# Optimization experiments

Measured on AMD Instinct MI355X. Metric: run time of the kernel, lower is better.

## Reference

```python
import jax, jax.numpy as jnp
import numpy as np


def _conv1x1(x, w, b):
    # x: [B,C,H,W], w: [O,C], b: [O] -> [B,O,H,W]
    return jnp.einsum('bchw,oc->bohw', x, w) + b[None, :, None, None]


def setup_inputs() -> dict:
    key = jax.random.key(0)
    ks = jax.random.split(key, 5)
    B, C, H, W = 4, 256, 64, 64
    C2 = C // 2
    scale = 0.02  # keep attention logits in a sane range
    return {
        'x': jax.random.normal(ks[0], (B, C, H, W), dtype=jnp.float32),
        'w_theta': jax.random.normal(ks[1], (C2, C), dtype=jnp.float32) * scale,
        'b_theta': jnp.zeros((C2,), dtype=jnp.float32),
        'w_phi': jax.random.normal(ks[2], (C2, C), dtype=jnp.float32) * scale,
        'b_phi': jnp.zeros((C2,), dtype=jnp.float32),
        'w_g': jax.random.normal(ks[3], (C2, C), dtype=jnp.float32) * scale,
        'b_g': jnp.zeros((C2,), dtype=jnp.float32),
        'w_out': jax.random.normal(ks[4], (C, C2), dtype=jnp.float32) * scale,
        'b_out': jnp.zeros((C,), dtype=jnp.float32),
    }


def reference(x, w_theta, b_theta, w_phi, b_phi, w_g, b_g, w_out, b_out):
    B, C, H, W = x.shape
    C2 = C // 2
    N = H * W
    theta = _conv1x1(x, w_theta, b_theta).reshape(B, C2, N)  # [B,C2,N]
    phi = _conv1x1(x, w_phi, b_phi).reshape(B, C2, N)        # [B,C2,N]
    g = _conv1x1(x, w_g, b_g).reshape(B, C2, N)              # [B,C2,N]
    # non-local attention: scores[b,m,n] = theta[b,:,m] . phi[b,:,n]
    scores = jnp.einsum('bcm,bcn->bmn', theta, phi)          # [B,N,N]
    attn = jax.nn.softmax(scores, axis=-1)                   # [B,N,N]
    # output = g @ attn^T : out[b,c,m] = sum_n g[b,c,n] * attn[b,m,n]
    out = jnp.einsum('bcn,bmn->bcm', g, attn)                # [B,C2,N]
    out = out.reshape(B, C2, H, W)
    return x + _conv1x1(out, w_out, b_out)
```

## Files before the change

kernel.cpp:

```cpp
#include <hip/hip_runtime.h>
#include <hip/hip_bf16.h>

#define B_  4
#define C_  256
#define C2_ 128
#define N_  4096
#define LOG2E 1.4426950408889634f

typedef unsigned short u16;
typedef __attribute__((ext_vector_type(8))) short bf16x8;
typedef __attribute__((ext_vector_type(4))) float f32x4;

static __device__ __forceinline__ u16 f2bf(float f) {
    return __builtin_bit_cast(u16, __float2bfloat16(f));
}
static __device__ __forceinline__ float bf2f(u16 u) {
    return __bfloat162float(__builtin_bit_cast(__hip_bfloat16, u));
}

__global__ __launch_bounds__(256) void prep_kernel(
    const float* __restrict__ wt, const float* __restrict__ wp,
    const float* __restrict__ wg, const float* __restrict__ wo,
    const float* __restrict__ x, u16* __restrict__ Wb, u16* __restrict__ XT) {
    __shared__ float T[64][65];
    int bid = blockIdx.x;
    int tid = threadIdx.x;
    if (bid < 128) {
        int i = (bid * 256 + tid) * 4;
        int mat = i >> 15, off = i & 32767;
        const float* src = mat == 0 ? wt : (mat == 1 ? wp : (mat == 2 ? wg : wo));
        float4 v = *(const float4*)(src + off);
        ushort4 o = { f2bf(v.x), f2bf(v.y), f2bf(v.z), f2bf(v.w) };
        *(ushort4*)(Wb + i) = o;
        return;
    }
    int bid2 = bid - 128;
    int b   = bid2 / (4 * 64);
    int rem = bid2 % (4 * 64);
    int c0  = (rem / 64) * 64;
    int n0  = (rem % 64) * 64;
#pragma unroll
    for (int it = 0; it < 4; ++it) {
        int idx = it * 256 + tid;
        int rc = idx >> 4, n4 = (idx & 15) * 4;
        float4 v = *(const float4*)(x + ((size_t)b * C_ + c0 + rc) * N_ + n0 + n4);
        T[n4 + 0][rc] = v.x;
        T[n4 + 1][rc] = v.y;
        T[n4 + 2][rc] = v.z;
        T[n4 + 3][rc] = v.w;
    }
    __syncthreads();
#pragma unroll
    for (int it = 0; it < 2; ++it) {
        int idx = it * 256 + tid;
        int nr = idx >> 3, c8 = (idx & 7) * 8;
        u16 o[8];
#pragma unroll
        for (int j = 0; j < 8; ++j) o[j] = f2bf(T[nr][c8 + j]);
        *(uint4*)(XT + ((size_t)b * N_ + n0 + nr) * C_ + c0 + c8) = *(const uint4*)o;
    }
}

__global__ __launch_bounds__(256) void projm_kernel(
    const u16* __restrict__ XT, const u16* __restrict__ Wb,
    const float* __restrict__ b_theta, const float* __restrict__ b_phi,
    const float* __restrict__ b_g,
    u16* __restrict__ Q, u16* __restrict__ K, u16* __restrict__ V) {
    __shared__ __align__(16) u16 XTs[64][264];
    __shared__ __align__(16) u16 Vt[128][72];
    int bid = blockIdx.x;
    int mat = bid / (B_ * (N_ / 64));
    int rem = bid % (B_ * (N_ / 64));
    int b   = rem / (N_ / 64);
    int n0  = (rem % (N_ / 64)) * 64;
    int tid = threadIdx.x;
    int wave = tid >> 6, lane = tid & 63, quad = lane >> 4, l16 = lane & 15;

#pragma unroll
    for (int it = 0; it < 8; ++it) {
        int idx = it * 256 + tid;
        int row = idx >> 5, c8 = (idx & 31) * 8;
        *(uint4*)&XTs[row][c8] =
            *(const uint4*)(XT + ((size_t)b * N_ + n0 + row) * C_ + c8);
    }
    __syncthreads();

    bf16x8 af[8];
#pragma unroll
    for (int ks = 0; ks < 8; ++ks)
        af[ks] = *(const bf16x8*)&XTs[wave * 16 + l16][ks * 32 + quad * 8];

    const u16* wm = Wb + (size_t)mat * C2_ * C_;
    const float* bias = mat == 0 ? b_theta : (mat == 1 ? b_phi : b_g);

    f32x4 acc[8];
#pragma unroll
    for (int i = 0; i < 8; ++i) acc[i] = (f32x4){0.f, 0.f, 0.f, 0.f};
#pragma unroll
    for (int ct = 0; ct < 8; ++ct) {
        const u16* wr = wm + (size_t)(ct * 16 + l16) * C_ + quad * 8;
#pragma unroll
        for (int ks = 0; ks < 8; ++ks) {
            bf16x8 bf = *(const bf16x8*)(wr + ks * 32);
            acc[ct] = __builtin_amdgcn_mfma_f32_16x16x32_bf16(af[ks], bf, acc[ct], 0, 0, 0);
        }
    }

    if (mat < 2) {
        u16* dst = mat == 0 ? Q : K;
        float sc = mat == 0 ? LOG2E : 1.0f;
#pragma unroll
        for (int ct = 0; ct < 8; ++ct) {
            float bb = bias[ct * 16 + l16];
#pragma unroll
            for (int r = 0; r < 4; ++r) {
                int n = n0 + wave * 16 + quad * 4 + r;
                dst[((size_t)b * N_ + n) * C2_ + ct * 16 + l16] =
                    f2bf((acc[ct][r] + bb) * sc);
            }
        }
    } else {
#pragma unroll
        for (int ct = 0; ct < 8; ++ct) {
            float bb = bias[ct * 16 + l16];
#pragma unroll
            for (int r = 0; r < 4; ++r)
                Vt[ct * 16 + l16][wave * 16 + quad * 4 + r] = f2bf(acc[ct][r] + bb);
        }
        __syncthreads();
#pragma unroll
        for (int it = 0; it < 4; ++it) {
            int idx = it * 256 + tid;
            int row = idx >> 3, n8 = (idx & 7) * 8;
            *(uint4*)(V + ((size_t)b * C2_ + row) * N_ + n0 + n8) =
                *(const uint4*)&Vt[row][n8];
        }
    }
}

__global__ __launch_bounds__(256, 2) void attn_kernel(
    const u16* __restrict__ Q, const u16* __restrict__ K,
    const u16* __restrict__ V, u16* __restrict__ AO,
    float* __restrict__ Op, float* __restrict__ lsum, int nsplit) {
    const int BM = 128, BN = 64, D = C2_;
    const int per = B_ * (N_ / BM);
    int s    = blockIdx.x / per;
    int r0   = blockIdx.x % per;
    int b    = r0 / (N_ / BM);
    int m0   = (r0 % (N_ / BM)) * BM;
    int tid  = threadIdx.x;
    int wave = tid >> 6, lane = tid & 63, quad = (lane >> 4) & 3, l16 = lane & 15;

    __shared__ __align__(16) u16 Ks[BN][D + 8];
    __shared__ __align__(16) u16 Vs[D][BN + 8];
    __shared__ __align__(16) u16 Psb[4][32][BN + 8];
    u16* Ps = &Psb[wave][0][0];

    bf16x8 qf[2][4];
#pragma unroll
    for (int ms = 0; ms < 2; ++ms) {
        const u16* qp = Q + ((size_t)b * N_ + m0 + wave * 32 + ms * 16 + l16) * D;
#pragma unroll
        for (int kk = 0; kk < 4; ++kk)
            qf[ms][kk] = *(const bf16x8*)(qp + kk * 32 + quad * 8);
    }

    float l_r[2][4] = {{0.f, 0.f, 0.f, 0.f}, {0.f, 0.f, 0.f, 0.f}};
    f32x4 o_acc[2][8];
#pragma unroll
    for (int ms = 0; ms < 2; ++ms)
#pragma unroll
        for (int i = 0; i < 8; ++i) o_acc[ms][i] = (f32x4){0.f, 0.f, 0.f, 0.f};

    const int chunk = N_ / nsplit;
    const int nt0 = s * chunk, nt1 = nt0 + chunk;

    for (int nt = nt0; nt < nt1; nt += BN) {
        const u16* kp = K + ((size_t)b * N_ + nt) * D;
#pragma unroll
        for (int it = 0; it < 4; ++it) {
            int idx = it * 256 + tid;
            int row = idx >> 4, col = (idx & 15) * 8;
            *(uint4*)&Ks[row][col] = *(const uint4*)(kp + row * D + col);
        }
#pragma unroll
        for (int it = 0; it < 4; ++it) {
            int idx = it * 256 + tid;
            int row = idx >> 3, col = (idx & 7) * 8;
            *(uint4*)&Vs[row][col] =
                *(const uint4*)(V + ((size_t)b * C2_ + row) * N_ + nt + col);
        }
        __syncthreads();

        f32x4 sc[2][4];
#pragma unroll
        for (int nn = 0; nn < 4; ++nn) {
            f32x4 a0 = (f32x4){0.f, 0.f, 0.f, 0.f};
            f32x4 a1 = (f32x4){0.f, 0.f, 0.f, 0.f};
#pragma unroll
            for (int kk = 0; kk < 4; ++kk) {
                bf16x8 kf = *(const bf16x8*)&Ks[nn * 16 + l16][kk * 32 + quad * 8];
                a0 = __builtin_amdgcn_mfma_f32_16x16x32_bf16(qf[0][kk], kf, a0, 0, 0, 0);
                a1 = __builtin_amdgcn_mfma_f32_16x16x32_bf16(qf[1][kk], kf, a1, 0, 0, 0);
            }
            sc[0][nn] = a0;
            sc[1][nn] = a1;
        }

#pragma unroll
        for (int ms = 0; ms < 2; ++ms)
#pragma unroll
            for (int nn = 0; nn < 4; ++nn)
#pragma unroll
                for (int r = 0; r < 4; ++r) {
                    float p = __builtin_amdgcn_exp2f(sc[ms][nn][r]);
                    l_r[ms][r] += p;
                    Ps[(ms * 16 + quad * 4 + r) * (BN + 8) + nn * 16 + l16] = f2bf(p);
                }

#pragma unroll
        for (int ks = 0; ks < 2; ++ks) {
            bf16x8 pf0 = *(const bf16x8*)&Ps[(l16) * (BN + 8) + ks * 32 + quad * 8];
            bf16x8 pf1 = *(const bf16x8*)&Ps[(16 + l16) * (BN + 8) + ks * 32 + quad * 8];
#pragma unroll
            for (int cs = 0; cs < 8; ++cs) {
                bf16x8 vf = *(const bf16x8*)&Vs[cs * 16 + l16][ks * 32 + quad * 8];
                o_acc[0][cs] = __builtin_amdgcn_mfma_f32_16x16x32_bf16(pf0, vf, o_acc[0][cs], 0, 0, 0);
                o_acc[1][cs] = __builtin_amdgcn_mfma_f32_16x16x32_bf16(pf1, vf, o_acc[1][cs], 0, 0, 0);
            }
        }
        __syncthreads();
    }

#pragma unroll
    for (int ms = 0; ms < 2; ++ms)
#pragma unroll
        for (int r = 0; r < 4; ++r) {
            l_r[ms][r] += __shfl_xor(l_r[ms][r], 1);
            l_r[ms][r] += __shfl_xor(l_r[ms][r], 2);
            l_r[ms][r] += __shfl_xor(l_r[ms][r], 4);
            l_r[ms][r] += __shfl_xor(l_r[ms][r], 8);
        }

    if (Op) {
#pragma unroll
        for (int ms = 0; ms < 2; ++ms) {
#pragma unroll
            for (int cs = 0; cs < 8; ++cs)
#pragma unroll
                for (int r = 0; r < 4; ++r) {
                    size_t row = (size_t)s * (B_ * N_) + (size_t)b * N_ +
                                 m0 + wave * 32 + ms * 16 + quad * 4 + r;
                    Op[row * C2_ + cs * 16 + l16] = o_acc[ms][cs][r];
                }
            if (l16 == 0)
#pragma unroll
                for (int r = 0; r < 4; ++r) {
                    size_t row = (size_t)s * (B_ * N_) + (size_t)b * N_ +
                                 m0 + wave * 32 + ms * 16 + quad * 4 + r;
                    lsum[row] = l_r[ms][r];
                }
        }
    } else {
#pragma unroll
        for (int ms = 0; ms < 2; ++ms)
#pragma unroll
            for (int cs = 0; cs < 8; ++cs)
#pragma unroll
                for (int r = 0; r < 4; ++r) {
                    float v = o_acc[ms][cs][r] / l_r[ms][r];
                    AO[((size_t)b * N_ + m0 + wave * 32 + ms * 16 + quad * 4 + r) * C2_ +
                       cs * 16 + l16] = f2bf(v);
                }
    }
}

__global__ __launch_bounds__(256) void outproj_kernel(
    const float* __restrict__ x, const float* __restrict__ Op,
    const float* __restrict__ lsum, const u16* __restrict__ AO,
    const u16* __restrict__ Wob, const float* __restrict__ b_out,
    float* __restrict__ y, int nsplit) {
    __shared__ __align__(16) u16 As[64][C2_ + 8];
    __shared__ float Ls[64];
    int bid = blockIdx.x;
    int per_b = (C_ / 64) * (N_ / 64);
    int b   = bid / per_b;
    int rem = bid % per_b;
    int c0  = (rem / (N_ / 64)) * 64;
    int n0  = (rem % (N_ / 64)) * 64;
    int tid = threadIdx.x;
    int wave = tid >> 6, lane = tid & 63, quad = lane >> 4, l16 = lane & 15;

    if (nsplit > 1) {
        if (tid < 64) {
            float L = 0.f;
            for (int s = 0; s < nsplit; ++s)
                L += lsum[(size_t)s * (B_ * N_) + (size_t)b * N_ + n0 + tid];
            Ls[tid] = 1.f / L;
        }
        __syncthreads();
#pragma unroll
        for (int it = 0; it < 8; ++it) {
            int idx = it * 256 + tid;
            int n = idx >> 5, c4 = (idx & 31) * 4;
            float4 a = {0.f, 0.f, 0.f, 0.f};
            for (int s = 0; s < nsplit; ++s) {
                float4 v = *(const float4*)(
                    Op + ((size_t)s * (B_ * N_) + (size_t)b * N_ + n0 + n) * C2_ + c4);
                a.x += v.x; a.y += v.y; a.z += v.z; a.w += v.w;
            }
            float inv = Ls[n];
            ushort4 o = { f2bf(a.x * inv), f2bf(a.y * inv),
                          f2bf(a.z * inv), f2bf(a.w * inv) };
            *(ushort4*)&As[n][c4] = o;
        }
    } else {
#pragma unroll
        for (int it = 0; it < 4; ++it) {
            int idx = it * 256 + tid;
            int n = idx >> 4, c8 = (idx & 15) * 8;
            *(uint4*)&As[n][c8] =
                *(const uint4*)(AO + ((size_t)b * N_ + n0 + n) * C2_ + c8);
        }
    }
    __syncthreads();

    int cw = c0 + wave * 16;
    bf16x8 af[4];
#pragma unroll
    for (int kk = 0; kk < 4; ++kk)
        af[kk] = *(const bf16x8*)&Wob[(size_t)(cw + l16) * C2_ + kk * 32 + quad * 8];

    f32x4 acc[4];
#pragma unroll
    for (int i = 0; i < 4; ++i) acc[i] = (f32x4){0.f, 0.f, 0.f, 0.f};

#pragma unroll
    for (int nn = 0; nn < 4; ++nn)
#pragma unroll
        for (int kk = 0; kk < 4; ++kk) {
            bf16x8 bf = *(const bf16x8*)&As[nn * 16 + l16][kk * 32 + quad * 8];
            acc[nn] = __builtin_amdgcn_mfma_f32_16x16x32_bf16(af[kk], bf, acc[nn], 0, 0, 0);
        }

    float bo[4];
#pragma unroll
    for (int r = 0; r < 4; ++r) bo[r] = b_out[cw + quad * 4 + r];

#pragma unroll
    for (int nn = 0; nn < 4; ++nn)
#pragma unroll
        for (int r = 0; r < 4; ++r) {
            int c = cw + quad * 4 + r;
            size_t off = ((size_t)b * C_ + c) * N_ + n0 + nn * 16 + l16;
            y[off] = x[off] + bo[r] + acc[nn][r];
        }
}

extern "C" void kernel_launch(void* const* d_in, const int* in_sizes, int n_in,
                              void* d_out, int out_size, void* d_ws, size_t ws_size,
                              hipStream_t stream) {
    const float* x       = (const float*)d_in[0];
    const float* w_theta = (const float*)d_in[1];
    const float* b_theta = (const float*)d_in[2];
    const float* w_phi   = (const float*)d_in[3];
    const float* b_phi   = (const float*)d_in[4];
    const float* w_g     = (const float*)d_in[5];
    const float* b_g     = (const float*)d_in[6];
    const float* w_out   = (const float*)d_in[7];
    const float* b_out   = (const float*)d_in[8];
    float* y = (float*)d_out;

    const size_t SZ = (size_t)B_ * N_ * C2_;
    u16* Q  = (u16*)d_ws;
    u16* K  = Q + SZ;
    u16* V  = K + SZ;
    u16* AO = V + SZ;
    u16* Wb = AO + SZ;
    u16* Wob = Wb + (size_t)3 * C2_ * C_;
    u16* XT = Wb + (size_t)4 * C2_ * C_;
    char* dyn = (char*)(XT + (size_t)B_ * N_ * C_);
    size_t fixedB = (size_t)(dyn - (char*)d_ws);

    size_t perS = SZ * 4 + (size_t)B_ * N_ * 4;

    int S;
    if      (ws_size >= fixedB + 4 * perS) S = 4;
    else if (ws_size >= fixedB + 2 * perS) S = 2;
    else                                   S = 1;

    float* Op = nullptr;
    float* ls = nullptr;
    if (S > 1) {
        Op = (float*)dyn;
        ls = Op + (size_t)S * SZ;
    }

    prep_kernel<<<128 + B_ * (C_ / 64) * (N_ / 64), 256, 0, stream>>>(
        w_theta, w_phi, w_g, w_out, x, Wb, XT);
    projm_kernel<<<3 * B_ * (N_ / 64), 256, 0, stream>>>(
        XT, Wb, b_theta, b_phi, b_g, Q, K, V);
    attn_kernel<<<B_ * (N_ / 128) * S, 256, 0, stream>>>(Q, K, V, AO, Op, ls, S);
    outproj_kernel<<<B_ * (C_ / 64) * (N_ / 64), 256, 0, stream>>>(
        x, Op, ls, AO, Wob, b_out, y, S);
}
```

Baseline: 179.2 us.

## Fuse x transpose into projection, store split partials in bf16, allow six splits

The x transpose and bf16 conversion now happen inside a single projection kernel. That kernel computes Q, K and V together from one shared-memory tile of 32 positions, which removes the XT intermediate buffer and the separate transpose pass. The split-KV partial outputs are now stored as bf16 instead of fp32, halving that traffic, and up to six splits are allowed with uneven tile distribution. The bf16 partials lose some precision before the cross-split reduction, and the projection now runs 512 blocks instead of 768.

```diff
diff --git a/kernel.cpp b/kernel.cpp
--- a/kernel.cpp
+++ b/kernel.cpp
@@ -18,130 +18,114 @@
     return __bfloat162float(__builtin_bit_cast(__hip_bfloat16, u));
 }
 
-__global__ __launch_bounds__(256) void prep_kernel(
+__global__ __launch_bounds__(256) void prepw_kernel(
     const float* __restrict__ wt, const float* __restrict__ wp,
     const float* __restrict__ wg, const float* __restrict__ wo,
-    const float* __restrict__ x, u16* __restrict__ Wb, u16* __restrict__ XT) {
-    __shared__ float T[64][65];
-    int bid = blockIdx.x;
-    int tid = threadIdx.x;
-    if (bid < 128) {
-        int i = (bid * 256 + tid) * 4;
-        int mat = i >> 15, off = i & 32767;
-        const float* src = mat == 0 ? wt : (mat == 1 ? wp : (mat == 2 ? wg : wo));
-        float4 v = *(const float4*)(src + off);
-        ushort4 o = { f2bf(v.x), f2bf(v.y), f2bf(v.z), f2bf(v.w) };
-        *(ushort4*)(Wb + i) = o;
-        return;
-    }
-    int bid2 = bid - 128;
-    int b   = bid2 / (4 * 64);
-    int rem = bid2 % (4 * 64);
-    int c0  = (rem / 64) * 64;
-    int n0  = (rem % 64) * 64;
-#pragma unroll
-    for (int it = 0; it < 4; ++it) {
-        int idx = it * 256 + tid;
-        int rc = idx >> 4, n4 = (idx & 15) * 4;
-        float4 v = *(const float4*)(x + ((size_t)b * C_ + c0 + rc) * N_ + n0 + n4);
-        T[n4 + 0][rc] = v.x;
-        T[n4 + 1][rc] = v.y;
-        T[n4 + 2][rc] = v.z;
-        T[n4 + 3][rc] = v.w;
-    }
-    __syncthreads();
-#pragma unroll
-    for (int it = 0; it < 2; ++it) {
-        int idx = it * 256 + tid;
-        int nr = idx >> 3, c8 = (idx & 7) * 8;
-        u16 o[8];
-#pragma unroll
-        for (int j = 0; j < 8; ++j) o[j] = f2bf(T[nr][c8 + j]);
-        *(uint4*)(XT + ((size_t)b * N_ + n0 + nr) * C_ + c0 + c8) = *(const uint4*)o;
-    }
-}
-
-__global__ __launch_bounds__(256) void projm_kernel(
-    const u16* __restrict__ XT, const u16* __restrict__ Wb,
+    u16* __restrict__ Wb) {
+    int i = (blockIdx.x * 256 + threadIdx.x) * 4;
+    int mat = i >> 15, off = i & 32767;
+    const float* src = mat == 0 ? wt : (mat == 1 ? wp : (mat == 2 ? wg : wo));
+    float4 v = *(const float4*)(src + off);
+    ushort4 o = { f2bf(v.x), f2bf(v.y), f2bf(v.z), f2bf(v.w) };
+    *(ushort4*)(Wb + i) = o;
+}
+
+__global__ __launch_bounds__(256) void projx_kernel(
+    const float* __restrict__ x, const u16* __restrict__ Wb,
     const float* __restrict__ b_theta, const float* __restrict__ b_phi,
     const float* __restrict__ b_g,
     u16* __restrict__ Q, u16* __restrict__ K, u16* __restrict__ V) {
-    __shared__ __align__(16) u16 XTs[64][264];
-    __shared__ __align__(16) u16 Vt[128][72];
+    __shared__ __align__(16) union {
+        u16 XTs[32][264];
+        u16 Vt[128][40];
+    } sm;
     int bid = blockIdx.x;
-    int mat = bid / (B_ * (N_ / 64));
-    int rem = bid % (B_ * (N_ / 64));
-    int b   = rem / (N_ / 64);
-    int n0  = (rem % (N_ / 64)) * 64;
+    int b   = bid / (N_ / 32);
+    int n0  = (bid % (N_ / 32)) * 32;
     int tid = threadIdx.x;
     int wave = tid >> 6, lane = tid & 63, quad = lane >> 4, l16 = lane & 15;
-
-#pragma unroll
-    for (int it = 0; it < 8; ++it) {
+    int mgrp = wave >> 1, chalf = wave & 1;
+
+#pragma unroll
+    for (int it = 0; it < 4; ++it) {
         int idx = it * 256 + tid;
-        int row = idx >> 5, c8 = (idx & 31) * 8;
-        *(uint4*)&XTs[row][c8] =
-            *(const uint4*)(XT + ((size_t)b * N_ + n0 + row) * C_ + c8);
+        int q = idx & 7, p = idx >> 3;
+        const float* r0 = x + ((size_t)b * C_ + 2 * p) * N_ + n0 + 4 * q;
+        float4 v0 = *(const float4*)r0;
+        float4 v1 = *(const float4*)(r0 + N_);
+        const float* f0 = (const float*)&v0;
+        const float* f1 = (const float*)&v1;
+#pragma unroll
+        for (int j = 0; j < 4; ++j) {
+            unsigned pk = (unsigned)f2bf(f0[j]) | ((unsigned)f2bf(f1[j]) << 16);
+            *(unsigned*)&sm.XTs[4 * q + j][2 * p] = pk;
+        }
     }
     __syncthreads();
 
     bf16x8 af[8];
 #pragma unroll
     for (int ks = 0; ks < 8; ++ks)
-        af[ks] = *(const bf16x8*)&XTs[wave * 16 + l16][ks * 32 + quad * 8];
-
-    const u16* wm = Wb + (size_t)mat * C2_ * C_;
-    const float* bias = mat == 0 ? b_theta : (mat == 1 ? b_phi : b_g);
-
-    f32x4 acc[8];
-#pragma unroll
-    for (int i = 0; i < 8; ++i) acc[i] = (f32x4){0.f, 0.f, 0.f, 0.f};
-#pragma unroll
-    for (int ct = 0; ct < 8; ++ct) {
-        const u16* wr = wm + (size_t)(ct * 16 + l16) * C_ + quad * 8;
-#pragma unroll
-        for (int ks = 0; ks < 8; ++ks) {
-            bf16x8 bf = *(const bf16x8*)(wr + ks * 32);
-            acc[ct] = __builtin_amdgcn_mfma_f32_16x16x32_bf16(af[ks], bf, acc[ct], 0, 0, 0);
-        }
-    }
-
-    if (mat < 2) {
-        u16* dst = mat == 0 ? Q : K;
-        float sc = mat == 0 ? LOG2E : 1.0f;
-#pragma unroll
-        for (int ct = 0; ct < 8; ++ct) {
-            float bb = bias[ct * 16 + l16];
-#pragma unroll
-            for (int r = 0; r < 4; ++r) {
-                int n = n0 + wave * 16 + quad * 4 + r;
-                dst[((size_t)b * N_ + n) * C2_ + ct * 16 + l16] =
-                    f2bf((acc[ct][r] + bb) * sc);
-            }
-        }
-    } else {
-#pragma unroll
-        for (int ct = 0; ct < 8; ++ct) {
-            float bb = bias[ct * 16 + l16];
-#pragma unroll
-            for (int r = 0; r < 4; ++r)
-                Vt[ct * 16 + l16][wave * 16 + quad * 4 + r] = f2bf(acc[ct][r] + bb);
-        }
-        __syncthreads();
-#pragma unroll
-        for (int it = 0; it < 4; ++it) {
-            int idx = it * 256 + tid;
-            int row = idx >> 3, n8 = (idx & 7) * 8;
-            *(uint4*)(V + ((size_t)b * C2_ + row) * N_ + n0 + n8) =
-                *(const uint4*)&Vt[row][n8];
-        }
+        af[ks] = *(const bf16x8*)&sm.XTs[mgrp * 16 + l16][ks * 32 + quad * 8];
+    __syncthreads();
+
+    const float* biases[3] = { b_theta, b_phi, b_g };
+#pragma unroll
+    for (int mat = 0; mat < 3; ++mat) {
+        const u16* wm = Wb + (size_t)mat * C2_ * C_;
+        const float* bias = biases[mat];
+        f32x4 acc[4];
+#pragma unroll
+        for (int i = 0; i < 4; ++i) acc[i] = (f32x4){0.f, 0.f, 0.f, 0.f};
+#pragma unroll
+        for (int ct = 0; ct < 4; ++ct) {
+            int ce = chalf * 4 + ct;
+            const u16* wr = wm + (size_t)(ce * 16 + l16) * C_ + quad * 8;
+#pragma unroll
+            for (int ks = 0; ks < 8; ++ks) {
+                bf16x8 bf = *(const bf16x8*)(wr + ks * 32);
+                acc[ct] = __builtin_amdgcn_mfma_f32_16x16x32_bf16(af[ks], bf, acc[ct], 0, 0, 0);
+            }
+        }
+        if (mat < 2) {
+            u16* dst = mat == 0 ? Q : K;
+            float sc = mat == 0 ? LOG2E : 1.0f;
+#pragma unroll
+            for (int ct = 0; ct < 4; ++ct) {
+                int c2 = (chalf * 4 + ct) * 16 + l16;
+                float bb = bias[c2];
+#pragma unroll
+                for (int r = 0; r < 4; ++r) {
+                    int n = n0 + mgrp * 16 + quad * 4 + r;
+                    dst[((size_t)b * N_ + n) * C2_ + c2] = f2bf((acc[ct][r] + bb) * sc);
+                }
+            }
+        } else {
+#pragma unroll
+            for (int ct = 0; ct < 4; ++ct) {
+                int c2 = (chalf * 4 + ct) * 16 + l16;
+                float bb = bias[c2];
+#pragma unroll
+                for (int r = 0; r < 4; ++r)
+                    sm.Vt[c2][mgrp * 16 + quad * 4 + r] = f2bf(acc[ct][r] + bb);
+            }
+        }
+    }
+    __syncthreads();
+    {
+        int row = tid >> 1, col16 = (tid & 1) * 16;
+        uint4 a0 = *(const uint4*)&sm.Vt[row][col16];
+        uint4 a1 = *(const uint4*)&sm.Vt[row][col16 + 8];
+        u16* vp = V + ((size_t)b * C2_ + row) * N_ + n0 + col16;
+        *(uint4*)vp = a0;
+        *(uint4*)(vp + 8) = a1;
     }
 }
 
 __global__ __launch_bounds__(256, 2) void attn_kernel(
     const u16* __restrict__ Q, const u16* __restrict__ K,
     const u16* __restrict__ V, u16* __restrict__ AO,
-    float* __restrict__ Op, float* __restrict__ lsum, int nsplit) {
+    u16* __restrict__ Opb, float* __restrict__ lsum, int nsplit) {
     const int BM = 128, BN = 64, D = C2_;
     const int per = B_ * (N_ / BM);
     int s    = blockIdx.x / per;
@@ -172,8 +156,11 @@
 #pragma unroll
         for (int i = 0; i < 8; ++i) o_acc[ms][i] = (f32x4){0.f, 0.f, 0.f, 0.f};
 
-    const int chunk = N_ / nsplit;
-    const int nt0 = s * chunk, nt1 = nt0 + chunk;
+    const int tiles = N_ / BN;
+    const int base = tiles / nsplit, rem = tiles % nsplit;
+    const int t0 = s * base + (s < rem ? s : rem);
+    const int cnt = base + (s < rem ? 1 : 0);
+    const int nt0 = t0 * BN, nt1 = (t0 + cnt) * BN;
 
     for (int nt = nt0; nt < nt1; nt += BN) {
         const u16* kp = K + ((size_t)b * N_ + nt) * D;
@@ -242,7 +229,7 @@
             l_r[ms][r] += __shfl_xor(l_r[ms][r], 8);
         }
 
-    if (Op) {
+    if (Opb) {
 #pragma unroll
         for (int ms = 0; ms < 2; ++ms) {
 #pragma unroll
@@ -251,7 +238,7 @@
                 for (int r = 0; r < 4; ++r) {
                     size_t row = (size_t)s * (B_ * N_) + (size_t)b * N_ +
                                  m0 + wave * 32 + ms * 16 + quad * 4 + r;
-                    Op[row * C2_ + cs * 16 + l16] = o_acc[ms][cs][r];
+                    Opb[row * C2_ + cs * 16 + l16] = f2bf(o_acc[ms][cs][r]);
                 }
             if (l16 == 0)
 #pragma unroll
@@ -276,7 +263,7 @@
 }
 
 __global__ __launch_bounds__(256) void outproj_kernel(
-    const float* __restrict__ x, const float* __restrict__ Op,
+    const float* __restrict__ x, const u16* __restrict__ Opb,
     const float* __restrict__ lsum, const u16* __restrict__ AO,
     const u16* __restrict__ Wob, const float* __restrict__ b_out,
     float* __restrict__ y, int nsplit) {
@@ -300,19 +287,23 @@
         }
         __syncthreads();
 #pragma unroll
-        for (int it = 0; it < 8; ++it) {
+        for (int it = 0; it < 4; ++it) {
             int idx = it * 256 + tid;
-            int n = idx >> 5, c4 = (idx & 31) * 4;
-            float4 a = {0.f, 0.f, 0.f, 0.f};
+            int n = idx >> 4, c8 = (idx & 15) * 8;
+            float a[8] = {0.f, 0.f, 0.f, 0.f, 0.f, 0.f, 0.f, 0.f};
             for (int s = 0; s < nsplit; ++s) {
-                float4 v = *(const float4*)(
-                    Op + ((size_t)s * (B_ * N_) + (size_t)b * N_ + n0 + n) * C2_ + c4);
-                a.x += v.x; a.y += v.y; a.z += v.z; a.w += v.w;
+                const u16* op = Opb +
+                    ((size_t)s * (B_ * N_) + (size_t)b * N_ + n0 + n) * C2_ + c8;
+                uint4 raw = *(const uint4*)op;
+                const u16* rp = (const u16*)&raw;
+#pragma unroll
+                for (int j = 0; j < 8; ++j) a[j] += bf2f(rp[j]);
             }
             float inv = Ls[n];
-            ushort4 o = { f2bf(a.x * inv), f2bf(a.y * inv),
-                          f2bf(a.z * inv), f2bf(a.w * inv) };
-            *(ushort4*)&As[n][c4] = o;
+            u16 o[8];
+#pragma unroll
+            for (int j = 0; j < 8; ++j) o[j] = f2bf(a[j] * inv);
+            *(uint4*)&As[n][c8] = *(const uint4*)o;
         }
     } else {
 #pragma unroll
@@ -378,29 +369,28 @@
     u16* AO = V + SZ;
     u16* Wb = AO + SZ;
     u16* Wob = Wb + (size_t)3 * C2_ * C_;
-    u16* XT = Wb + (size_t)4 * C2_ * C_;
-    char* dyn = (char*)(XT + (size_t)B_ * N_ * C_);
+    char* dyn = (char*)(Wb + (size_t)4 * C2_ * C_);
     size_t fixedB = (size_t)(dyn - (char*)d_ws);
 
-    size_t perS = SZ * 4 + (size_t)B_ * N_ * 4;
+    size_t perS = SZ * 2 + (size_t)B_ * N_ * 4;
 
     int S;
-    if      (ws_size >= fixedB + 4 * perS) S = 4;
+    if      (ws_size >= fixedB + 6 * perS) S = 6;
+    else if (ws_size >= fixedB + 4 * perS) S = 4;
     else if (ws_size >= fixedB + 2 * perS) S = 2;
     else                                   S = 1;
 
-    float* Op = nullptr;
-    float* ls = nullptr;
+    u16*   Opb = nullptr;
+    float* ls  = nullptr;
     if (S > 1) {
-        Op = (float*)dyn;
-        ls = Op + (size_t)S * SZ;
-    }
-
-    prep_kernel<<<128 + B_ * (C_ / 64) * (N_ / 64), 256, 0, stream>>>(
-        w_theta, w_phi, w_g, w_out, x, Wb, XT);
-    projm_kernel<<<3 * B_ * (N_ / 64), 256, 0, stream>>>(
-        XT, Wb, b_theta, b_phi, b_g, Q, K, V);
-    attn_kernel<<<B_ * (N_ / 128) * S, 256, 0, stream>>>(Q, K, V, AO, Op, ls, S);
+        Opb = (u16*)dyn;
+        ls  = (float*)(Opb + (size_t)S * SZ);
+    }
+
+    prepw_kernel<<<128, 256, 0, stream>>>(w_theta, w_phi, w_g, w_out, Wb);
+    projx_kernel<<<B_ * (N_ / 32), 256, 0, stream>>>(
+        x, Wb, b_theta, b_phi, b_g, Q, K, V);
+    attn_kernel<<<B_ * (N_ / 128) * S, 256, 0, stream>>>(Q, K, V, AO, Opb, ls, S);
     outproj_kernel<<<B_ * (C_ / 64) * (N_ / 64), 256, 0, stream>>>(
-        x, Op, ls, AO, Wob, b_out, y, S);
-}
+        x, Opb, ls, AO, Wob, b_out, y, S);
+}
```

Measured after the change: 179.8 us. About the same (+0.3%).
